# Optimization experiments

Measured on AMD Instinct MI355X. Metric: run time of the kernel, lower is better.

## Reference

```python
import jax, jax.numpy as jnp
import numpy as np

B, S, D = 4, 2048, 1024


def setup_inputs() -> dict:
    key = jax.random.key(0)
    ks = jax.random.split(key, 9)
    s = 1.0 / np.sqrt(D)
    return {
        "x": jax.random.normal(ks[0], (B, S, D), dtype=jnp.float32),
        "Wq": jax.random.normal(ks[1], (D, D), dtype=jnp.float32) * s,
        "bq": jnp.zeros((D,), dtype=jnp.float32),
        "Wk": jax.random.normal(ks[2], (D, D), dtype=jnp.float32) * s,
        "bk": jnp.zeros((D,), dtype=jnp.float32),
        "Wv": jax.random.normal(ks[3], (D, D), dtype=jnp.float32) * s,
        "bv": jnp.zeros((D,), dtype=jnp.float32),
        "Wo": jax.random.normal(ks[4], (D, D), dtype=jnp.float32) * s,
        "bo": jnp.zeros((D,), dtype=jnp.float32),
    }


def reference(x, Wq, bq, Wk, bk, Wv, bv, Wo, bo):
    # Projections: [B,S,D] @ [D,D] -> [B,S,D]
    q = jnp.einsum("bsd,de->bse", x, Wq) + bq
    k = jnp.einsum("bsd,de->bse", x, Wk) + bk
    v = jnp.einsum("bsd,de->bse", x, Wv) + bv
    # Unscaled single-head attention: scores [B,S,S]
    scores = jnp.einsum("bqd,bkd->bqk", q, k)
    dist = jax.nn.softmax(scores, axis=-1)
    attn = jnp.einsum("bqk,bkd->bqd", dist, v)
    # Output projection + residual
    return jnp.einsum("bsd,de->bse", attn, Wo) + bo + x
```

## Files before the change

### kernel.cpp

```cpp
#include <hip/hip_runtime.h>
#include <hip/hip_bf16.h>

#define DEVI __device__ __forceinline__

typedef __attribute__((ext_vector_type(8))) _Float16 f16x8;
typedef __attribute__((ext_vector_type(4))) float f32x4;
typedef __attribute__((ext_vector_type(4))) unsigned short us4;

DEVI unsigned short f2h(float f) {
  union { _Float16 h; unsigned short u; } v;
  v.h = (_Float16)f;
  return v.u;
}

__global__ void __launch_bounds__(256) k_convert_f16(
    const float* __restrict__ x, unsigned short* __restrict__ o, int n4) {
  int i = blockIdx.x * 256 + threadIdx.x;
  if (i >= n4) return;
  float4 v = reinterpret_cast<const float4*>(x)[i];
  us4 h;
  h[0] = f2h(v.x); h[1] = f2h(v.y); h[2] = f2h(v.z); h[3] = f2h(v.w);
  reinterpret_cast<us4*>(o)[i] = h;
}

__global__ void __launch_bounds__(256) k_transpose_f16(
    const float* __restrict__ W, unsigned short* __restrict__ T, int n) {
  __shared__ float t[32][33];
  int tx = threadIdx.x & 31, ty = threadIdx.x >> 5;
  int n0 = blockIdx.x * 32, k0 = blockIdx.y * 32;
#pragma unroll
  for (int r = 0; r < 4; ++r)
    t[ty + r * 8][tx] = W[(size_t)(k0 + ty + r * 8) * n + n0 + tx];
  __syncthreads();
#pragma unroll
  for (int r = 0; r < 4; ++r) {
    int nn = n0 + ty + r * 8;
    T[(size_t)nn * n + k0 + tx] = f2h(t[tx][ty + r * 8]);
  }
}

DEVI void stage_tile64(unsigned short* lbase, const unsigned short* g, int ldg,
                       int wid, int lane) {
#pragma unroll
  for (int it = 0; it < 4; ++it) {
    int chunk = it * 256 + wid * 64 + lane;
    int r = chunk >> 3, s = chunk & 7;
    int c = (s ^ (r & 7)) * 8;
    const unsigned short* gp = g + (size_t)r * ldg + c;
    unsigned short* lp = lbase + (it * 256 + wid * 64) * 8;
    __builtin_amdgcn_global_load_lds(
        (const __attribute__((address_space(1))) unsigned int*)gp,
        (__attribute__((address_space(3))) unsigned int*)lp, 16, 0, 0);
  }
}

DEVI f16x8 frag(const unsigned short* base, int row, int kk, int lr) {
  int slot = (kk * 4 + lr) ^ (row & 7);
  return *reinterpret_cast<const f16x8*>(base + row * 64 + slot * 8);
}

template <int EPI>
__global__ void __launch_bounds__(256, 4) k_gemm(
    const unsigned short* __restrict__ A, const unsigned short* __restrict__ B,
    int K, int ldA, int ldB,
    size_t azs, size_t bzs, size_t czs,
    const float* __restrict__ bias, const float* __restrict__ resid,
    float* __restrict__ outF, unsigned short* __restrict__ outH, int ldc) {
  __shared__ unsigned short lds[2 * 8192];
  unsigned short* Alds = lds;
  unsigned short* Blds = lds + 8192;

  const int gx = gridDim.x, gy = gridDim.y;
  const int nwg = gx * gy * gridDim.z;
  const int l = (blockIdx.z * gy + blockIdx.y) * gx + blockIdx.x;
  const int nl = (l & 7) * (nwg >> 3) + (l >> 3);
  const int bx = nl % gx;
  const int rem = nl / gx;
  const int by = rem % gy;
  const int z = rem / gy;

  const int tid = threadIdx.x, lane = tid & 63, wid = tid >> 6;
  const int wr = (wid >> 1) * 64, wc = (wid & 1) * 64;
  const int lc = lane & 15, lr = lane >> 4;
  const size_t row0 = (size_t)bx * 128, col0 = (size_t)by * 128;

  const unsigned short* Ag = A + (size_t)z * azs + row0 * ldA;
  const unsigned short* Bg = B + (size_t)z * bzs + col0 * ldB;

  f32x4 acc[4][4] = {};

  for (int k0 = 0; k0 < K; k0 += 64) {
    stage_tile64(Alds, Ag + k0, ldA, wid, lane);
    stage_tile64(Blds, Bg + k0, ldB, wid, lane);
    __syncthreads();
#pragma unroll
    for (int kk = 0; kk < 2; ++kk) {
      f16x8 af[4], bf[4];
#pragma unroll
      for (int i = 0; i < 4; ++i) {
        af[i] = frag(Alds, wr + i * 16 + lc, kk, lr);
        bf[i] = frag(Blds, wc + i * 16 + lc, kk, lr);
      }
#pragma unroll
      for (int mi = 0; mi < 4; ++mi)
#pragma unroll
        for (int ni = 0; ni < 4; ++ni)
          acc[mi][ni] = __builtin_amdgcn_mfma_f32_16x16x32_f16(af[mi], bf[ni], acc[mi][ni], 0, 0, 0);
    }
    __syncthreads();
  }

#pragma unroll
  for (int mi = 0; mi < 4; ++mi) {
#pragma unroll
    for (int ni = 0; ni < 4; ++ni) {
      const int r0 = (int)row0 + wr + mi * 16 + lr * 4;
      const int c = (int)col0 + wc + ni * 16 + lc;
      f32x4 a = acc[mi][ni];
      if (EPI == 0) {
        float b = bias[c];
#pragma unroll
        for (int r = 0; r < 4; ++r)
          outH[(size_t)(r0 + r) * ldc + c] = f2h(a[r] + b);
      } else if (EPI == 1) {
        float b = bias[c];
        us4 pk;
#pragma unroll
        for (int r = 0; r < 4; ++r) pk[r] = f2h(a[r] + b);
        *reinterpret_cast<us4*>(outH + ((size_t)(r0 >> 11) * 1024 + c) * 2048 + (r0 & 2047)) = pk;
      } else if (EPI == 2) {
#pragma unroll
        for (int r = 0; r < 4; ++r)
          outF[(size_t)z * czs + (size_t)(r0 + r) * ldc + c] = a[r];
      } else if (EPI == 3) {
#pragma unroll
        for (int r = 0; r < 4; ++r)
          outH[(size_t)z * czs + (size_t)(r0 + r) * ldc + c] = f2h(a[r]);
      } else {
        float b = bias[c];
#pragma unroll
        for (int r = 0; r < 4; ++r) {
          size_t idx = (size_t)(r0 + r) * ldc + c;
          outF[idx] = a[r] + b + resid[idx];
        }
      }
    }
  }
}

__global__ void __launch_bounds__(256) k_softmax(
    const float* __restrict__ S, unsigned short* __restrict__ P) {
  __shared__ float red[4];
  const int row = blockIdx.x, tid = threadIdx.x;
  const int lane = tid & 63, wid = tid >> 6;
  const float* src = S + (size_t)row * 2048;
  float4 v0 = *reinterpret_cast<const float4*>(src + tid * 8);
  float4 v1 = *reinterpret_cast<const float4*>(src + tid * 8 + 4);
  float vv[8] = {v0.x, v0.y, v0.z, v0.w, v1.x, v1.y, v1.z, v1.w};
  float m = vv[0];
#pragma unroll
  for (int j = 1; j < 8; ++j) m = fmaxf(m, vv[j]);
#pragma unroll
  for (int o = 32; o > 0; o >>= 1) m = fmaxf(m, __shfl_xor(m, o));
  if (lane == 0) red[wid] = m;
  __syncthreads();
  m = fmaxf(fmaxf(red[0], red[1]), fmaxf(red[2], red[3]));
  __syncthreads();
  float e[8];
  float s = 0.f;
#pragma unroll
  for (int j = 0; j < 8; ++j) { e[j] = __expf(vv[j] - m); s += e[j]; }
#pragma unroll
  for (int o = 32; o > 0; o >>= 1) s += __shfl_xor(s, o);
  if (lane == 0) red[wid] = s;
  __syncthreads();
  s = red[0] + red[1] + red[2] + red[3];
  float inv = 1.0f / s;
  us4 p0, p1;
#pragma unroll
  for (int j = 0; j < 4; ++j) p0[j] = f2h(e[j] * inv);
#pragma unroll
  for (int j = 0; j < 4; ++j) p1[j] = f2h(e[j + 4] * inv);
  us4* dst = reinterpret_cast<us4*>(P + (size_t)row * 4096 + tid * 8);
  dst[0] = p0;
  dst[1] = p1;
}

extern "C" void kernel_launch(void* const* d_in, const int* in_sizes, int n_in,
                              void* d_out, int out_size, void* d_ws, size_t ws_size,
                              hipStream_t stream) {
  (void)in_sizes; (void)n_in; (void)out_size;
  const float* x  = (const float*)d_in[0];
  const float* Wq = (const float*)d_in[1];
  const float* bq = (const float*)d_in[2];
  const float* Wk = (const float*)d_in[3];
  const float* bk = (const float*)d_in[4];
  const float* Wv = (const float*)d_in[5];
  const float* bv = (const float*)d_in[6];
  const float* Wo = (const float*)d_in[7];
  const float* bo = (const float*)d_in[8];
  float* out = (float*)d_out;

  char* p = (char*)d_ws;
  size_t used = 0;
  auto take = [&](size_t bytes) {
    char* r = p;
    size_t pad = (bytes + 255) & ~(size_t)255;
    p += pad;
    used += pad;
    return r;
  };
  const size_t SD = (size_t)4 * 2048 * 1024;
  unsigned short* x_h  = (unsigned short*)take(SD * 2);
  unsigned short* q_h  = (unsigned short*)take(SD * 2);
  unsigned short* k_h  = (unsigned short*)take(SD * 2);
  unsigned short* WqT  = (unsigned short*)take((size_t)1024 * 1024 * 2);
  unsigned short* WkT  = (unsigned short*)take((size_t)1024 * 1024 * 2);
  unsigned short* WvT  = (unsigned short*)take((size_t)1024 * 1024 * 2);
  unsigned short* WoT  = (unsigned short*)take((size_t)1024 * 1024 * 2);
  unsigned short* v_t  = (unsigned short*)take(SD * 2);
  unsigned short* attn = (unsigned short*)take(SD * 2);
  const size_t SC_B = (size_t)2048 * 2048;
  int nz = (ws_size - used >= 4 * SC_B * 4 + 4096) ? 4 : 1;
  float* scores = (float*)take((size_t)nz * SC_B * 4);

  dim3 blk(256);
  k_convert_f16<<<dim3(8192), blk, 0, stream>>>(x, x_h, (int)(SD / 4));
  k_transpose_f16<<<dim3(32, 32), blk, 0, stream>>>(Wq, WqT, 1024);
  k_transpose_f16<<<dim3(32, 32), blk, 0, stream>>>(Wk, WkT, 1024);
  k_transpose_f16<<<dim3(32, 32), blk, 0, stream>>>(Wv, WvT, 1024);
  k_transpose_f16<<<dim3(32, 32), blk, 0, stream>>>(Wo, WoT, 1024);

  k_gemm<0><<<dim3(64, 8, 1), blk, 0, stream>>>(
      x_h, WqT, 1024, 1024, 1024, 0, 0, 0, bq, nullptr, nullptr, q_h, 1024);
  k_gemm<0><<<dim3(64, 8, 1), blk, 0, stream>>>(
      x_h, WkT, 1024, 1024, 1024, 0, 0, 0, bk, nullptr, nullptr, k_h, 1024);
  k_gemm<1><<<dim3(64, 8, 1), blk, 0, stream>>>(
      x_h, WvT, 1024, 1024, 1024, 0, 0, 0, bv, nullptr, nullptr, v_t, 2048);

  const size_t QZS = (size_t)2048 * 1024;
  const size_t VZS = (size_t)1024 * 2048;
  const size_t PZS = SC_B * 2;
  for (int b0 = 0; b0 < 4; b0 += nz) {
    const size_t oq = (size_t)b0 * QZS;
    k_gemm<2><<<dim3(16, 16, nz), blk, 0, stream>>>(
        q_h + oq, k_h + oq, 1024, 1024, 1024,
        QZS, QZS, SC_B, nullptr, nullptr, scores, nullptr, 2048);
    k_softmax<<<dim3(2048 * nz), blk, 0, stream>>>(scores, (unsigned short*)scores);
    k_gemm<3><<<dim3(16, 8, nz), blk, 0, stream>>>(
        (const unsigned short*)scores, v_t + (size_t)b0 * VZS,
        2048, 4096, 2048, PZS, VZS, QZS,
        nullptr, nullptr, nullptr, attn + oq, 1024);
  }
  k_gemm<4><<<dim3(64, 8, 1), blk, 0, stream>>>(
      attn, WoT, 1024, 1024, 1024, 0, 0, 0, bo, x, out, nullptr, 1024);
}
```

Measured before the change: 230.2 us.

## Triple-buffer GEMM staging, enlarge tiles to 256x128, fuse QKV projections

The GEMM kernel now uses 512-thread blocks with 256x128 output tiles and a three-stage LDS ring. Async global-to-LDS loads for tile t+2 are issued while tile t is computed, gated by explicit vmcnt waits and raw barriers, so global load latency overlaps the MFMA work. The Q, K and V projections are merged into one launch over a concatenated transposed weight, with the epilogue routing each column range to its own output. The workspace fallback for a smaller score buffer is dropped and all batches run in one launch. The larger tiles and 144KB of LDS limit occupancy and reduce the number of blocks.

After: 232.3 us. About the same (+0.9%).

```diff
diff --git a/kernel.cpp b/kernel.cpp
--- a/kernel.cpp
+++ b/kernel.cpp
@@ -6,6 +6,13 @@
 typedef __attribute__((ext_vector_type(8))) _Float16 f16x8;
 typedef __attribute__((ext_vector_type(4))) float f32x4;
 typedef __attribute__((ext_vector_type(4))) unsigned short us4;
+
+#define VMW(N) asm volatile("s_waitcnt vmcnt(" #N ")" ::: "memory")
+DEVI void sbar() {
+  asm volatile("" ::: "memory");
+  __builtin_amdgcn_s_barrier();
+  asm volatile("" ::: "memory");
+}
 
 DEVI unsigned short f2h(float f) {
   union { _Float16 h; unsigned short u; } v;
@@ -39,20 +46,32 @@
   }
 }
 
-DEVI void stage_tile64(unsigned short* lbase, const unsigned short* g, int ldg,
-                       int wid, int lane) {
+DEVI void stageA(unsigned short* lbase, const unsigned short* g, int ldg, int tid) {
 #pragma unroll
   for (int it = 0; it < 4; ++it) {
-    int chunk = it * 256 + wid * 64 + lane;
+    int chunk = it * 512 + tid;
     int r = chunk >> 3, s = chunk & 7;
     int c = (s ^ (r & 7)) * 8;
     const unsigned short* gp = g + (size_t)r * ldg + c;
-    unsigned short* lp = lbase + (it * 256 + wid * 64) * 8;
+    unsigned short* lp = lbase + (it * 512 + (tid & ~63)) * 8;
     __builtin_amdgcn_global_load_lds(
         (const __attribute__((address_space(1))) unsigned int*)gp,
         (__attribute__((address_space(3))) unsigned int*)lp, 16, 0, 0);
   }
 }
+DEVI void stageB(unsigned short* lbase, const unsigned short* g, int ldg, int tid) {
+#pragma unroll
+  for (int it = 0; it < 2; ++it) {
+    int chunk = it * 512 + tid;
+    int r = chunk >> 3, s = chunk & 7;
+    int c = (s ^ (r & 7)) * 8;
+    const unsigned short* gp = g + (size_t)r * ldg + c;
+    unsigned short* lp = lbase + (it * 512 + (tid & ~63)) * 8;
+    __builtin_amdgcn_global_load_lds(
+        (const __attribute__((address_space(1))) unsigned int*)gp,
+        (__attribute__((address_space(3))) unsigned int*)lp, 16, 0, 0);
+  }
+}
 
 DEVI f16x8 frag(const unsigned short* base, int row, int kk, int lr) {
   int slot = (kk * 4 + lr) ^ (row & 7);
@@ -60,15 +79,15 @@
 }
 
 template <int EPI>
-__global__ void __launch_bounds__(256, 4) k_gemm(
+__global__ void __launch_bounds__(512, 2) k_gemm(
     const unsigned short* __restrict__ A, const unsigned short* __restrict__ B,
-    int K, int ldA, int ldB,
+    int nt, int ldA, int ldB,
     size_t azs, size_t bzs, size_t czs,
-    const float* __restrict__ bias, const float* __restrict__ resid,
-    float* __restrict__ outF, unsigned short* __restrict__ outH, int ldc) {
-  __shared__ unsigned short lds[2 * 8192];
-  unsigned short* Alds = lds;
-  unsigned short* Blds = lds + 8192;
+    const float* __restrict__ b0, const float* __restrict__ b1,
+    const float* __restrict__ b2, const float* __restrict__ resid,
+    float* __restrict__ outF, unsigned short* __restrict__ o0,
+    unsigned short* __restrict__ o1, unsigned short* __restrict__ o2, int ldc) {
+  __shared__ unsigned short lds[3 * 24576];
 
   const int gx = gridDim.x, gy = gridDim.y;
   const int nwg = gx * gy * gridDim.z;
@@ -82,24 +101,38 @@
   const int tid = threadIdx.x, lane = tid & 63, wid = tid >> 6;
   const int wr = (wid >> 1) * 64, wc = (wid & 1) * 64;
   const int lc = lane & 15, lr = lane >> 4;
-  const size_t row0 = (size_t)bx * 128, col0 = (size_t)by * 128;
+  const size_t row0 = (size_t)bx * 256, col0 = (size_t)by * 128;
 
   const unsigned short* Ag = A + (size_t)z * azs + row0 * ldA;
   const unsigned short* Bg = B + (size_t)z * bzs + col0 * ldB;
 
   f32x4 acc[4][4] = {};
 
-  for (int k0 = 0; k0 < K; k0 += 64) {
-    stage_tile64(Alds, Ag + k0, ldA, wid, lane);
-    stage_tile64(Blds, Bg + k0, ldB, wid, lane);
-    __syncthreads();
+  stageA(lds, Ag, ldA, tid);
+  stageB(lds + 16384, Bg, ldB, tid);
+  stageA(lds + 24576, Ag + 64, ldA, tid);
+  stageB(lds + 24576 + 16384, Bg + 64, ldB, tid);
+
+  for (int t = 0; t < nt; ++t) {
+    unsigned short* cur = lds + (t % 3) * 24576;
+    if (t + 2 < nt) {
+      unsigned short* nx = lds + ((t + 2) % 3) * 24576;
+      stageA(nx, Ag + (size_t)(t + 2) * 64, ldA, tid);
+      stageB(nx + 16384, Bg + (size_t)(t + 2) * 64, ldB, tid);
+      VMW(12);
+    } else if (t + 1 < nt) {
+      VMW(6);
+    } else {
+      VMW(0);
+    }
+    sbar();
 #pragma unroll
     for (int kk = 0; kk < 2; ++kk) {
       f16x8 af[4], bf[4];
 #pragma unroll
       for (int i = 0; i < 4; ++i) {
-        af[i] = frag(Alds, wr + i * 16 + lc, kk, lr);
-        bf[i] = frag(Blds, wc + i * 16 + lc, kk, lr);
+        af[i] = frag(cur, wr + i * 16 + lc, kk, lr);
+        bf[i] = frag(cur + 16384, wc + i * 16 + lc, kk, lr);
       }
 #pragma unroll
       for (int mi = 0; mi < 4; ++mi)
@@ -107,7 +140,7 @@
         for (int ni = 0; ni < 4; ++ni)
           acc[mi][ni] = __builtin_amdgcn_mfma_f32_16x16x32_f16(af[mi], bf[ni], acc[mi][ni], 0, 0, 0);
     }
-    __syncthreads();
+    sbar();
   }
 
 #pragma unroll
@@ -118,16 +151,25 @@
       const int c = (int)col0 + wc + ni * 16 + lc;
       f32x4 a = acc[mi][ni];
       if (EPI == 0) {
-        float b = bias[c];
-#pragma unroll
-        for (int r = 0; r < 4; ++r)
-          outH[(size_t)(r0 + r) * ldc + c] = f2h(a[r] + b);
-      } else if (EPI == 1) {
-        float b = bias[c];
-        us4 pk;
-#pragma unroll
-        for (int r = 0; r < 4; ++r) pk[r] = f2h(a[r] + b);
-        *reinterpret_cast<us4*>(outH + ((size_t)(r0 >> 11) * 1024 + c) * 2048 + (r0 & 2047)) = pk;
+        const int sub = (int)(col0 >> 10);
+        const int cc = c & 1023;
+        if (sub == 0) {
+          float b = b0[cc];
+#pragma unroll
+          for (int r = 0; r < 4; ++r)
+            o0[(size_t)(r0 + r) * 1024 + cc] = f2h(a[r] + b);
+        } else if (sub == 1) {
+          float b = b1[cc];
+#pragma unroll
+          for (int r = 0; r < 4; ++r)
+            o1[(size_t)(r0 + r) * 1024 + cc] = f2h(a[r] + b);
+        } else {
+          float b = b2[cc];
+          us4 pk;
+#pragma unroll
+          for (int r = 0; r < 4; ++r) pk[r] = f2h(a[r] + b);
+          *reinterpret_cast<us4*>(o2 + ((size_t)(r0 >> 11) * 1024 + cc) * 2048 + (r0 & 2047)) = pk;
+        }
       } else if (EPI == 2) {
 #pragma unroll
         for (int r = 0; r < 4; ++r)
@@ -135,9 +177,9 @@
       } else if (EPI == 3) {
 #pragma unroll
         for (int r = 0; r < 4; ++r)
-          outH[(size_t)z * czs + (size_t)(r0 + r) * ldc + c] = f2h(a[r]);
+          o0[(size_t)z * czs + (size_t)(r0 + r) * ldc + c] = f2h(a[r]);
       } else {
-        float b = bias[c];
+        float b = b0[c];
 #pragma unroll
         for (int r = 0; r < 4; ++r) {
           size_t idx = (size_t)(r0 + r) * ldc + c;
@@ -189,7 +231,7 @@
 extern "C" void kernel_launch(void* const* d_in, const int* in_sizes, int n_in,
                               void* d_out, int out_size, void* d_ws, size_t ws_size,
                               hipStream_t stream) {
-  (void)in_sizes; (void)n_in; (void)out_size;
+  (void)in_sizes; (void)n_in; (void)out_size; (void)ws_size;
   const float* x  = (const float*)d_in[0];
   const float* Wq = (const float*)d_in[1];
   const float* bq = (const float*)d_in[2];
@@ -202,56 +244,44 @@
   float* out = (float*)d_out;
 
   char* p = (char*)d_ws;
-  size_t used = 0;
   auto take = [&](size_t bytes) {
     char* r = p;
-    size_t pad = (bytes + 255) & ~(size_t)255;
-    p += pad;
-    used += pad;
+    p += (bytes + 255) & ~(size_t)255;
     return r;
   };
   const size_t SD = (size_t)4 * 2048 * 1024;
-  unsigned short* x_h  = (unsigned short*)take(SD * 2);
-  unsigned short* q_h  = (unsigned short*)take(SD * 2);
-  unsigned short* k_h  = (unsigned short*)take(SD * 2);
-  unsigned short* WqT  = (unsigned short*)take((size_t)1024 * 1024 * 2);
-  unsigned short* WkT  = (unsigned short*)take((size_t)1024 * 1024 * 2);
-  unsigned short* WvT  = (unsigned short*)take((size_t)1024 * 1024 * 2);
-  unsigned short* WoT  = (unsigned short*)take((size_t)1024 * 1024 * 2);
-  unsigned short* v_t  = (unsigned short*)take(SD * 2);
-  unsigned short* attn = (unsigned short*)take(SD * 2);
+  unsigned short* x_h   = (unsigned short*)take(SD * 2);
+  unsigned short* q_h   = (unsigned short*)take(SD * 2);
+  unsigned short* k_h   = (unsigned short*)take(SD * 2);
+  unsigned short* WqkvT = (unsigned short*)take((size_t)3072 * 1024 * 2);
+  unsigned short* WoT   = (unsigned short*)take((size_t)1024 * 1024 * 2);
+  unsigned short* v_t   = (unsigned short*)take(SD * 2);
+  unsigned short* attn  = (unsigned short*)take(SD * 2);
   const size_t SC_B = (size_t)2048 * 2048;
-  int nz = (ws_size - used >= 4 * SC_B * 4 + 4096) ? 4 : 1;
-  float* scores = (float*)take((size_t)nz * SC_B * 4);
-
-  dim3 blk(256);
+  float* scores = (float*)take(4 * SC_B * 4);
+
+  dim3 blk(256), blk5(512);
   k_convert_f16<<<dim3(8192), blk, 0, stream>>>(x, x_h, (int)(SD / 4));
-  k_transpose_f16<<<dim3(32, 32), blk, 0, stream>>>(Wq, WqT, 1024);
-  k_transpose_f16<<<dim3(32, 32), blk, 0, stream>>>(Wk, WkT, 1024);
-  k_transpose_f16<<<dim3(32, 32), blk, 0, stream>>>(Wv, WvT, 1024);
+  k_transpose_f16<<<dim3(32, 32), blk, 0, stream>>>(Wq, WqkvT, 1024);
+  k_transpose_f16<<<dim3(32, 32), blk, 0, stream>>>(Wk, WqkvT + (size_t)1024 * 1024, 1024);
+  k_transpose_f16<<<dim3(32, 32), blk, 0, stream>>>(Wv, WqkvT + (size_t)2048 * 1024, 1024);
   k_transpose_f16<<<dim3(32, 32), blk, 0, stream>>>(Wo, WoT, 1024);
 
-  k_gemm<0><<<dim3(64, 8, 1), blk, 0, stream>>>(
-      x_h, WqT, 1024, 1024, 1024, 0, 0, 0, bq, nullptr, nullptr, q_h, 1024);
-  k_gemm<0><<<dim3(64, 8, 1), blk, 0, stream>>>(
-      x_h, WkT, 1024, 1024, 1024, 0, 0, 0, bk, nullptr, nullptr, k_h, 1024);
-  k_gemm<1><<<dim3(64, 8, 1), blk, 0, stream>>>(
-      x_h, WvT, 1024, 1024, 1024, 0, 0, 0, bv, nullptr, nullptr, v_t, 2048);
+  k_gemm<0><<<dim3(32, 24, 1), blk5, 0, stream>>>(
+      x_h, WqkvT, 16, 1024, 1024, 0, 0, 0,
+      bq, bk, bv, nullptr, nullptr, q_h, k_h, v_t, 0);
 
   const size_t QZS = (size_t)2048 * 1024;
   const size_t VZS = (size_t)1024 * 2048;
   const size_t PZS = SC_B * 2;
-  for (int b0 = 0; b0 < 4; b0 += nz) {
-    const size_t oq = (size_t)b0 * QZS;
-    k_gemm<2><<<dim3(16, 16, nz), blk, 0, stream>>>(
-        q_h + oq, k_h + oq, 1024, 1024, 1024,
-        QZS, QZS, SC_B, nullptr, nullptr, scores, nullptr, 2048);
-    k_softmax<<<dim3(2048 * nz), blk, 0, stream>>>(scores, (unsigned short*)scores);
-    k_gemm<3><<<dim3(16, 8, nz), blk, 0, stream>>>(
-        (const unsigned short*)scores, v_t + (size_t)b0 * VZS,
-        2048, 4096, 2048, PZS, VZS, QZS,
-        nullptr, nullptr, nullptr, attn + oq, 1024);
-  }
-  k_gemm<4><<<dim3(64, 8, 1), blk, 0, stream>>>(
-      attn, WoT, 1024, 1024, 1024, 0, 0, 0, bo, x, out, nullptr, 1024);
-}
+  k_gemm<2><<<dim3(8, 16, 4), blk5, 0, stream>>>(
+      q_h, k_h, 16, 1024, 1024, QZS, QZS, SC_B,
+      nullptr, nullptr, nullptr, nullptr, scores, nullptr, nullptr, nullptr, 2048);
+  k_softmax<<<dim3(8192), blk, 0, stream>>>(scores, (unsigned short*)scores);
+  k_gemm<3><<<dim3(8, 8, 4), blk5, 0, stream>>>(
+      (const unsigned short*)scores, v_t, 32, 4096, 2048, PZS, VZS, QZS,
+      nullptr, nullptr, nullptr, nullptr, nullptr, attn, nullptr, nullptr, 1024);
+  k_gemm<4><<<dim3(32, 8, 1), blk5, 0, stream>>>(
+      attn, WoT, 16, 1024, 1024, 0, 0, 0,
+      bo, nullptr, nullptr, x, out, nullptr, nullptr, nullptr, 1024);
+}
```
